# Kernel optimization log

Measured on AMD Instinct MI355X. Metric: run time of the kernel, lower is better.

The kernel has to match this reference:

```python
import jax, jax.numpy as jnp
import numpy as np

THRESHOLD = 0.1  # clamped into [0.01, 0.5] as in the torch module

def setup_inputs() -> dict:
    key = jax.random.key(0)
    x = jax.random.normal(key, (16, 256, 8192), dtype=jnp.float32)  # (B, C, T)
    return {"x": x}

def reference(x):
    th = jnp.float32(min(max(THRESHOLD, 0.01), 0.5))
    B, C, T = x.shape
    xt = jnp.transpose(x, (2, 0, 1))  # (T, B, C) for scan over time

    def step(recon, cur):
        err = cur - recon
        net = (err > th).astype(x.dtype) - (err < -th).astype(x.dtype)
        return recon + net * th, net

    _, spikes_t = jax.lax.scan(step, jnp.zeros((B, C), dtype=x.dtype), xt)
    return jnp.transpose(spikes_t, (1, 2, 0))  # (B, C, T)
```

## Files before the change

### kernel.cpp

```cpp
#include <hip/hip_runtime.h>


constexpr int T    = 8192;
constexpr int NCH  = 4096;
constexpr int CPB  = 16;
constexpr int NBLK = NCH / CPB;

#define STEP(X,S) \
  "v_sub_f32 v48, v" #X ", v33\n\t"             \
  "v_med3_f32 v49, v48, v30, v31\n\t"           \
  "v_sub_f32 v48, v48, v49\n\t"                 \
  "v_mul_f32 v49, s11, v48\n\t"                 \
  "v_med3_f32 v" #S ", v49, -1.0, 1.0\n\t"      \
  "v_fma_f32 v33, v" #S ", s8, v33\n\t"

#define SLOT_CLOB(Q0,Q1,Q2,Q3,P0,P1,P2,P3) \
  "memory","s8","s11","v30","v31","v33","v48","v49", \
  "v" #Q0,"v" #Q1,"v" #Q2,"v" #Q3,"v" #P0,"v" #P1,"v" #P2,"v" #P3

#define SLOT(Q0,Q1,Q2,Q3,P0,P1,P2,P3,OFFS,OFFL) asm volatile( \
  "s_waitcnt vmcnt(30)\n\t" \
  STEP(Q0,P0) STEP(Q1,P1) STEP(Q2,P2) STEP(Q3,P3) \
  "global_store_dwordx4 v40, v[" #P0 ":" #P3 "], %1 offset:" #OFFS "\n\t" \
  "global_load_dwordx4 v[" #Q0 ":" #Q3 "], v40, %0 offset:" #OFFL "\n\t" \
  :: "s"(xp), "s"(op) : SLOT_CLOB(Q0,Q1,Q2,Q3,P0,P1,P2,P3))

#define SLOTND(Q0,Q1,Q2,Q3,P0,P1,P2,P3,OFFS) asm volatile( \
  STEP(Q0,P0) STEP(Q1,P1) STEP(Q2,P2) STEP(Q3,P3) \
  "global_store_dwordx4 v40, v[" #P0 ":" #P3 "], %1 offset:" #OFFS "\n\t" \
  :: "s"(xp), "s"(op) : SLOT_CLOB(Q0,Q1,Q2,Q3,P0,P1,P2,P3))

__global__ __launch_bounds__(64, 1) void dm_scan(const float* __restrict__ x,
                                                 float* __restrict__ out) {
    const int lane = threadIdx.x;
    if (lane >= CPB) return;
    const int ch = blockIdx.x * CPB + lane;

    const float* xp = x;
    float*       op = out;
    unsigned off0 = (unsigned)ch * (unsigned)(T * 4);

    asm volatile(
        "s_mov_b32 s8, 0x3dcccccd\n\t"
        "s_mov_b32 s11, 0x7e800000\n\t"
        "v_mov_b32 v30, 0xbdcccccd\n\t"
        "v_mov_b32 v31, 0x3dcccccd\n\t"
        "v_mov_b32 v33, 0\n\t"
        "v_mov_b32 v40, %2\n\t"
        "global_load_dwordx4 v[64:67],   v40, %0\n\t"
        "global_load_dwordx4 v[68:71],   v40, %0 offset:16\n\t"
        "global_load_dwordx4 v[72:75],   v40, %0 offset:32\n\t"
        "global_load_dwordx4 v[76:79],   v40, %0 offset:48\n\t"
        "global_load_dwordx4 v[80:83],   v40, %0 offset:64\n\t"
        "global_load_dwordx4 v[84:87],   v40, %0 offset:80\n\t"
        "global_load_dwordx4 v[88:91],   v40, %0 offset:96\n\t"
        "global_load_dwordx4 v[92:95],   v40, %0 offset:112\n\t"
        "global_load_dwordx4 v[96:99],   v40, %0 offset:128\n\t"
        "global_load_dwordx4 v[100:103], v40, %0 offset:144\n\t"
        "global_load_dwordx4 v[104:107], v40, %0 offset:160\n\t"
        "global_load_dwordx4 v[108:111], v40, %0 offset:176\n\t"
        "global_load_dwordx4 v[112:115], v40, %0 offset:192\n\t"
        "global_load_dwordx4 v[116:119], v40, %0 offset:208\n\t"
        "global_load_dwordx4 v[120:123], v40, %0 offset:224\n\t"
        "global_load_dwordx4 v[124:127], v40, %0 offset:240\n\t"
        "s_waitcnt vmcnt(0)\n\t"
        :: "s"(xp), "s"(op), "v"(off0)
        : "memory","s8","s11",
          "v30","v31","v33","v40","v48","v49",
          "v64","v65","v66","v67","v68","v69","v70","v71",
          "v72","v73","v74","v75","v76","v77","v78","v79",
          "v80","v81","v82","v83","v84","v85","v86","v87",
          "v88","v89","v90","v91","v92","v93","v94","v95",
          "v96","v97","v98","v99","v100","v101","v102","v103",
          "v104","v105","v106","v107","v108","v109","v110","v111",
          "v112","v113","v114","v115","v116","v117","v118","v119",
          "v120","v121","v122","v123","v124","v125","v126","v127");

#pragma clang loop unroll(disable)
    for (int it = 0; it < 127; ++it) {
        SLOT( 64, 65, 66, 67, 128,129,130,131,   0, 256);
        SLOT( 68, 69, 70, 71, 132,133,134,135,  16, 272);
        SLOT( 72, 73, 74, 75, 136,137,138,139,  32, 288);
        SLOT( 76, 77, 78, 79, 140,141,142,143,  48, 304);
        SLOT( 80, 81, 82, 83, 144,145,146,147,  64, 320);
        SLOT( 84, 85, 86, 87, 148,149,150,151,  80, 336);
        SLOT( 88, 89, 90, 91, 152,153,154,155,  96, 352);
        SLOT( 92, 93, 94, 95, 156,157,158,159, 112, 368);
        SLOT( 96, 97, 98, 99, 160,161,162,163, 128, 384);
        SLOT(100,101,102,103, 164,165,166,167, 144, 400);
        SLOT(104,105,106,107, 168,169,170,171, 160, 416);
        SLOT(108,109,110,111, 172,173,174,175, 176, 432);
        SLOT(112,113,114,115, 176,177,178,179, 192, 448);
        SLOT(116,117,118,119, 180,181,182,183, 208, 464);
        SLOT(120,121,122,123, 184,185,186,187, 224, 480);
        SLOT(124,125,126,127, 188,189,190,191, 240, 496);
        asm volatile("v_add_u32 v40, 0x100, v40" ::: "v40");
    }

    asm volatile("s_waitcnt vmcnt(0)" ::: "memory");
    SLOTND( 64, 65, 66, 67, 128,129,130,131,   0);
    SLOTND( 68, 69, 70, 71, 132,133,134,135,  16);
    SLOTND( 72, 73, 74, 75, 136,137,138,139,  32);
    SLOTND( 76, 77, 78, 79, 140,141,142,143,  48);
    SLOTND( 80, 81, 82, 83, 144,145,146,147,  64);
    SLOTND( 84, 85, 86, 87, 148,149,150,151,  80);
    SLOTND( 88, 89, 90, 91, 152,153,154,155,  96);
    SLOTND( 92, 93, 94, 95, 156,157,158,159, 112);
    SLOTND( 96, 97, 98, 99, 160,161,162,163, 128);
    SLOTND(100,101,102,103, 164,165,166,167, 144);
    SLOTND(104,105,106,107, 168,169,170,171, 160);
    SLOTND(108,109,110,111, 172,173,174,175, 176);
    SLOTND(112,113,114,115, 176,177,178,179, 192);
    SLOTND(116,117,118,119, 180,181,182,183, 208);
    SLOTND(120,121,122,123, 184,185,186,187, 224);
    SLOTND(124,125,126,127, 188,189,190,191, 240);
}

extern "C" void kernel_launch(void* const* d_in, const int* in_sizes, int n_in,
                              void* d_out, int out_size, void* d_ws, size_t ws_size,
                              hipStream_t stream) {
    const float* x   = (const float*)d_in[0];
    float*       out = (float*)d_out;
    dm_scan<<<NBLK, 64, 0, stream>>>(x, out);
}
```

Baseline: 150.3 us.

## Shorten per-step spike math and batch vmcnt waits every four slots

Replaces the five-instruction ternary quantization (med3 clamp, subtract, scale, med3) with a three-instruction form: an fma on |err| scaled to push values past threshold to saturation, a med3 clamp to [0,1], and a bfi that copies the sign bit of the error. This shortens the serial dependency chain through the recon accumulator. The s_waitcnt is also issued only every fourth slot with a looser vmcnt, which cuts wait instructions but relies on the loads for the following three slots already having landed. The exactness of the new thresholding depends on the chosen constants, so behavior at values near the threshold could differ.

```diff
diff --git a/kernel.cpp b/kernel.cpp
--- a/kernel.cpp
+++ b/kernel.cpp
@@ -8,18 +8,23 @@
 
 #define STEP(X,S) \
   "v_sub_f32 v48, v" #X ", v33\n\t"             \
-  "v_med3_f32 v49, v48, v30, v31\n\t"           \
-  "v_sub_f32 v48, v48, v49\n\t"                 \
-  "v_mul_f32 v49, s11, v48\n\t"                 \
-  "v_med3_f32 v" #S ", v49, -1.0, 1.0\n\t"      \
+  "v_fma_f32 v49, |v48|, v30, v31\n\t"          \
+  "v_med3_f32 v49, v49, 0, 1.0\n\t"             \
+  "v_bfi_b32 v" #S ", s10, v48, v49\n\t"        \
   "v_fma_f32 v33, v" #S ", s8, v33\n\t"
 
 #define SLOT_CLOB(Q0,Q1,Q2,Q3,P0,P1,P2,P3) \
-  "memory","s8","s11","v30","v31","v33","v48","v49", \
+  "memory","s8","s10","v30","v31","v33","v48","v49", \
   "v" #Q0,"v" #Q1,"v" #Q2,"v" #Q3,"v" #P0,"v" #P1,"v" #P2,"v" #P3
 
-#define SLOT(Q0,Q1,Q2,Q3,P0,P1,P2,P3,OFFS,OFFL) asm volatile( \
-  "s_waitcnt vmcnt(30)\n\t" \
+#define SLOTW(Q0,Q1,Q2,Q3,P0,P1,P2,P3,OFFS,OFFL) asm volatile( \
+  "s_waitcnt vmcnt(24)\n\t" \
+  STEP(Q0,P0) STEP(Q1,P1) STEP(Q2,P2) STEP(Q3,P3) \
+  "global_store_dwordx4 v40, v[" #P0 ":" #P3 "], %1 offset:" #OFFS "\n\t" \
+  "global_load_dwordx4 v[" #Q0 ":" #Q3 "], v40, %0 offset:" #OFFL "\n\t" \
+  :: "s"(xp), "s"(op) : SLOT_CLOB(Q0,Q1,Q2,Q3,P0,P1,P2,P3))
+
+#define SLOTN(Q0,Q1,Q2,Q3,P0,P1,P2,P3,OFFS,OFFL) asm volatile( \
   STEP(Q0,P0) STEP(Q1,P1) STEP(Q2,P2) STEP(Q3,P3) \
   "global_store_dwordx4 v40, v[" #P0 ":" #P3 "], %1 offset:" #OFFS "\n\t" \
   "global_load_dwordx4 v[" #Q0 ":" #Q3 "], v40, %0 offset:" #OFFL "\n\t" \
@@ -42,9 +47,9 @@
 
     asm volatile(
         "s_mov_b32 s8, 0x3dcccccd\n\t"
-        "s_mov_b32 s11, 0x7e800000\n\t"
-        "v_mov_b32 v30, 0xbdcccccd\n\t"
-        "v_mov_b32 v31, 0x3dcccccd\n\t"
+        "s_mov_b32 s10, 0x80000000\n\t"
+        "v_mov_b32 v30, 0x7e800000\n\t"
+        "v_mov_b32 v31, 0xfccccccd\n\t"
         "v_mov_b32 v33, 0\n\t"
         "v_mov_b32 v40, %2\n\t"
         "global_load_dwordx4 v[64:67],   v40, %0\n\t"
@@ -65,7 +70,7 @@
         "global_load_dwordx4 v[124:127], v40, %0 offset:240\n\t"
         "s_waitcnt vmcnt(0)\n\t"
         :: "s"(xp), "s"(op), "v"(off0)
-        : "memory","s8","s11",
+        : "memory","s8","s10",
           "v30","v31","v33","v40","v48","v49",
           "v64","v65","v66","v67","v68","v69","v70","v71",
           "v72","v73","v74","v75","v76","v77","v78","v79",
@@ -78,22 +83,22 @@
 
 #pragma clang loop unroll(disable)
     for (int it = 0; it < 127; ++it) {
-        SLOT( 64, 65, 66, 67, 128,129,130,131,   0, 256);
-        SLOT( 68, 69, 70, 71, 132,133,134,135,  16, 272);
-        SLOT( 72, 73, 74, 75, 136,137,138,139,  32, 288);
-        SLOT( 76, 77, 78, 79, 140,141,142,143,  48, 304);
-        SLOT( 80, 81, 82, 83, 144,145,146,147,  64, 320);
-        SLOT( 84, 85, 86, 87, 148,149,150,151,  80, 336);
-        SLOT( 88, 89, 90, 91, 152,153,154,155,  96, 352);
-        SLOT( 92, 93, 94, 95, 156,157,158,159, 112, 368);
-        SLOT( 96, 97, 98, 99, 160,161,162,163, 128, 384);
-        SLOT(100,101,102,103, 164,165,166,167, 144, 400);
-        SLOT(104,105,106,107, 168,169,170,171, 160, 416);
-        SLOT(108,109,110,111, 172,173,174,175, 176, 432);
-        SLOT(112,113,114,115, 176,177,178,179, 192, 448);
-        SLOT(116,117,118,119, 180,181,182,183, 208, 464);
-        SLOT(120,121,122,123, 184,185,186,187, 224, 480);
-        SLOT(124,125,126,127, 188,189,190,191, 240, 496);
+        SLOTW( 64, 65, 66, 67, 128,129,130,131,   0, 256);
+        SLOTN( 68, 69, 70, 71, 132,133,134,135,  16, 272);
+        SLOTN( 72, 73, 74, 75, 136,137,138,139,  32, 288);
+        SLOTN( 76, 77, 78, 79, 140,141,142,143,  48, 304);
+        SLOTW( 80, 81, 82, 83, 144,145,146,147,  64, 320);
+        SLOTN( 84, 85, 86, 87, 148,149,150,151,  80, 336);
+        SLOTN( 88, 89, 90, 91, 152,153,154,155,  96, 352);
+        SLOTN( 92, 93, 94, 95, 156,157,158,159, 112, 368);
+        SLOTW( 96, 97, 98, 99, 160,161,162,163, 128, 384);
+        SLOTN(100,101,102,103, 164,165,166,167, 144, 400);
+        SLOTN(104,105,106,107, 168,169,170,171, 160, 416);
+        SLOTN(108,109,110,111, 172,173,174,175, 176, 432);
+        SLOTW(112,113,114,115, 176,177,178,179, 192, 448);
+        SLOTN(116,117,118,119, 180,181,182,183, 208, 464);
+        SLOTN(120,121,122,123, 184,185,186,187, 224, 480);
+        SLOTN(124,125,126,127, 188,189,190,191, 240, 496);
         asm volatile("v_add_u32 v40, 0x100, v40" ::: "v40");
     }
 
```

Result: faster. 127.7 us (-15.1%).
